# Kernel tuning notes

Hardware: AMD Instinct MI355X
Metric: run time of the kernel (lower is better)

Reference implementation:

```python
import jax, jax.numpy as jnp
import numpy as np

TAU = 0.25
VTH = 1.0
RESET = 0.0


def setup_inputs() -> dict:
    key = jax.random.key(0)
    B, T, U = 64, 256, 1024
    inputs = jax.random.normal(key, (B, T, U), dtype=jnp.float32)
    return {"inputs": inputs}


def reference(inputs):
    # inputs: (B, T, U). LIF recurrence over time with threshold + soft reset.
    dt = inputs.dtype
    tau = jnp.asarray(TAU, dt)
    vth = jnp.asarray(VTH, dt)
    reset = jnp.asarray(RESET, dt)

    def step(v, x_t):
        v = tau * v + (1.0 - tau) * x_t          # leaky integrate
        s = (v > vth).astype(dt)                  # fire
        v = v - s * vth + s * reset               # reset fired neurons
        return v, s

    B, T, U = inputs.shape
    v0 = jnp.zeros((B, U), dtype=dt)
    xs = jnp.swapaxes(inputs, 0, 1)               # (T, B, U)
    _, spikes = jax.lax.scan(step, v0, xs)        # (T, B, U)
    return jnp.swapaxes(spikes, 0, 1)             # (B, T, U)
```

## Files before the change

kernel.cpp:

```cpp
#include <hip/hip_runtime.h>


typedef float f32x2 __attribute__((ext_vector_type(2)));

constexpr int kB  = 64;
constexpr int kT  = 256;
constexpr int kU  = 1024;
constexpr int kU2 = kU / 2;
constexpr int kC  = 16;
constexpr int kNCH = kT / kC;

__global__ __launch_bounds__(128)
void lif_kernel(const float* __restrict__ x, float* __restrict__ out) {
    const int idx = blockIdx.x * blockDim.x + threadIdx.x;
    const int b   = idx >> 9;
    const int u2  = idx & (kU2 - 1);

    const size_t base2 = (size_t)b * kT * kU2 + u2;
    const f32x2* __restrict__ xp = reinterpret_cast<const f32x2*>(x) + base2;
    f32x2* __restrict__ op       = reinterpret_cast<f32x2*>(out) + base2;

    f32x2 buf[3][kC];

#pragma unroll
    for (int j = 0; j < kC; ++j)
        buf[0][j] = xp[(size_t)j * kU2];
#pragma unroll
    for (int j = 0; j < kC; ++j)
        buf[1][j] = xp[(size_t)(kC + j) * kU2];

    float v0 = 0.0f, v1 = 0.0f;

#pragma unroll
    for (int c = 0; c < kNCH; ++c) {
        if (c + 2 < kNCH) {
#pragma unroll
            for (int j = 0; j < kC; ++j)
                buf[(c + 2) % 3][j] = xp[(size_t)((c + 2) * kC + j) * kU2];
        }
#pragma unroll
        for (int j = 0; j < kC; ++j) {
            const f32x2 xx = buf[c % 3][j];

            const float a0 = __fmul_rn(0.25f, v0);
            const float m0 = __fmul_rn(0.75f, xx.x);
            v0 = __fadd_rn(a0, m0);
            const float s0 = (v0 > 1.0f) ? 1.0f : 0.0f;
            v0 = __fsub_rn(v0, s0);

            const float a1 = __fmul_rn(0.25f, v1);
            const float m1 = __fmul_rn(0.75f, xx.y);
            v1 = __fadd_rn(a1, m1);
            const float s1 = (v1 > 1.0f) ? 1.0f : 0.0f;
            v1 = __fsub_rn(v1, s1);

            f32x2 s;
            s.x = s0;
            s.y = s1;
            __builtin_nontemporal_store(s, &op[(size_t)(c * kC + j) * kU2]);
        }
    }
}

extern "C" void kernel_launch(void* const* d_in, const int* in_sizes, int n_in,
                              void* d_out, int out_size, void* d_ws, size_t ws_size,
                              hipStream_t stream) {
    const float* x = (const float*)d_in[0];
    float* out = (float*)d_out;

    const int nthreads = kB * kU2;
    const int block = 128;
    const int grid = nthreads / block;
    lif_kernel<<<grid, block, 0, stream>>>(x, out);
}
```

Baseline: 108.8 us.

## Split time axis into two segments with warm-up recomputation for parallelism

Splits the 256-step recurrence into two 128-step segments processed by separate blocks. The second segment restarts from zero state and runs a 64-step warm-up before writing output, relying on the leak factor 0.25 shrinking any state difference below fp32 resolution. This doubles the thread count to hide memory latency in a latency-bound scan. In exchange it reads about a quarter more input. Exactness now depends on the contraction of the recurrence rather than on a strict sequential scan.

```diff
diff --git a/kernel.cpp b/kernel.cpp
--- a/kernel.cpp
+++ b/kernel.cpp
@@ -3,40 +3,37 @@
 
 typedef float f32x2 __attribute__((ext_vector_type(2)));
 
-constexpr int kB  = 64;
-constexpr int kT  = 256;
-constexpr int kU  = 1024;
-constexpr int kU2 = kU / 2;
-constexpr int kC  = 16;
-constexpr int kNCH = kT / kC;
+constexpr int kB   = 64;
+constexpr int kT   = 256;
+constexpr int kU   = 1024;
+constexpr int kU2  = kU / 2;
+constexpr int kSeg = 128;
+constexpr int kWarm = 64;
+constexpr int kC   = 16;
 
-__global__ __launch_bounds__(128)
-void lif_kernel(const float* __restrict__ x, float* __restrict__ out) {
-    const int idx = blockIdx.x * blockDim.x + threadIdx.x;
-    const int b   = idx >> 9;
-    const int u2  = idx & (kU2 - 1);
-
-    const size_t base2 = (size_t)b * kT * kU2 + u2;
-    const f32x2* __restrict__ xp = reinterpret_cast<const f32x2*>(x) + base2;
-    f32x2* __restrict__ op       = reinterpret_cast<f32x2*>(out) + base2;
+template <int NWARM>
+__device__ __forceinline__ void run_chain(const f32x2* __restrict__ lp,
+                                          f32x2* __restrict__ op) {
+    constexpr int NSTEPS = NWARM + kSeg;
+    constexpr int NCH    = NSTEPS / kC;
 
     f32x2 buf[3][kC];
 
 #pragma unroll
     for (int j = 0; j < kC; ++j)
-        buf[0][j] = xp[(size_t)j * kU2];
+        buf[0][j] = lp[(size_t)j * kU2];
 #pragma unroll
     for (int j = 0; j < kC; ++j)
-        buf[1][j] = xp[(size_t)(kC + j) * kU2];
+        buf[1][j] = lp[(size_t)(kC + j) * kU2];
 
     float v0 = 0.0f, v1 = 0.0f;
 
 #pragma unroll
-    for (int c = 0; c < kNCH; ++c) {
-        if (c + 2 < kNCH) {
+    for (int c = 0; c < NCH; ++c) {
+        if (c + 2 < NCH) {
 #pragma unroll
             for (int j = 0; j < kC; ++j)
-                buf[(c + 2) % 3][j] = xp[(size_t)((c + 2) * kC + j) * kU2];
+                buf[(c + 2) % 3][j] = lp[(size_t)((c + 2) * kC + j) * kU2];
         }
 #pragma unroll
         for (int j = 0; j < kC; ++j) {
@@ -54,11 +51,34 @@
             const float s1 = (v1 > 1.0f) ? 1.0f : 0.0f;
             v1 = __fsub_rn(v1, s1);
 
-            f32x2 s;
-            s.x = s0;
-            s.y = s1;
-            __builtin_nontemporal_store(s, &op[(size_t)(c * kC + j) * kU2]);
+            const int t = c * kC + j;
+            if (t >= NWARM) {
+                f32x2 s;
+                s.x = s0;
+                s.y = s1;
+                __builtin_nontemporal_store(s, op + (size_t)(t - NWARM) * kU2);
+            }
         }
+    }
+}
+
+__global__ __launch_bounds__(64)
+void lif_kernel(const float* __restrict__ x, float* __restrict__ out) {
+    const int bid = blockIdx.x;
+    const int seg = bid >> 9;
+    const int idx = ((bid & 511) << 6) | threadIdx.x;
+    const int b   = idx >> 9;
+    const int u2  = idx & (kU2 - 1);
+
+    const size_t base2 = (size_t)b * kT * kU2 + u2;
+    const f32x2* __restrict__ xp = reinterpret_cast<const f32x2*>(x) + base2;
+    f32x2* __restrict__ op       = reinterpret_cast<f32x2*>(out) + base2;
+
+    if (seg == 0) {
+        run_chain<0>(xp, op);
+    } else {
+        run_chain<kWarm>(xp + (size_t)(kSeg - kWarm) * kU2,
+                         op + (size_t)kSeg * kU2);
     }
 }
 
@@ -68,8 +88,5 @@
     const float* x = (const float*)d_in[0];
     float* out = (float*)d_out;
 
-    const int nthreads = kB * kU2;
-    const int block = 128;
-    const int grid = nthreads / block;
-    lif_kernel<<<grid, block, 0, stream>>>(x, out);
+    lif_kernel<<<1024, 64, 0, stream>>>(x, out);
 }
```

New measurement: 107.8 us. About the same (-0.9%).
